# Kernel optimization log

Measured on AMD Instinct MI355X. Metric: run time of the kernel, lower is better.

The kernel has to match this reference:

```python
import jax, jax.numpy as jnp
import numpy as np

B = 65536   # batch
D = 15      # data_dim = 4**n_qubits - 1 (2 qubits)
DT = 0.01   # time step


def _pauli_s_const():
    # SU(4) structure constants from 2-qubit Pauli strings (identity excluded).
    I = np.eye(2, dtype=complex)
    X = np.array([[0, 1], [1, 0]], dtype=complex)
    Y = np.array([[0, -1j], [1j, 0]], dtype=complex)
    Z = np.array([[1, 0], [0, -1]], dtype=complex)
    sig = [I, X, Y, Z]
    P = np.stack([np.kron(a, b) for a in sig for b in sig][1:])  # [15,4,4]
    T = np.einsum('iab,jbc,kca->ijk', P, P, P)  # tr(Pi Pj Pk)
    f = (np.imag(T) / 4.0).astype(np.float32)  # antisymmetric
    d = (np.real(T) / 4.0).astype(np.float32)  # symmetric
    return f, d


def setup_inputs() -> dict:
    key = jax.random.key(0)
    ks = jax.random.split(key, 24)
    f, d = _pauli_s_const()

    def lin_w(k, o, i):
        return jax.random.normal(k, (o, i), jnp.float32) / np.sqrt(i)

    def lin_b(k, o):
        return 0.001 * jax.random.normal(k, (o,), jnp.float32)

    dims = [(2, 1), (4, 2), (4, 4), (D * D, 4)]
    inp = {
        't': jax.random.uniform(ks[0], (B,), jnp.float32),
        'x': jax.random.normal(ks[1], (B, D), jnp.float32),
        'omega': 0.001 * jax.random.normal(ks[2], (D,), jnp.float32),
        'f': jnp.asarray(f),
        'd': jnp.asarray(d),
    }
    kidx = 3
    for net in ('x', 'y'):
        for li, (o, i) in enumerate(dims, start=1):
            inp[f'w{net}{li}'] = lin_w(ks[kidx], o, i); kidx += 1
            inp[f'b{net}{li}'] = lin_b(ks[kidx], o); kidx += 1
    return inp


def _forward(t, x, wx1, bx1, wx2, bx2, wx3, bx3, wx4, bx4,
             wy1, by1, wy2, by2, wy3, by3, wy4, by4, omega, f, d):
    t1 = t[:, None]  # [B,1]

    def mlp(w1, b1, w2, b2, w3, b3, w4, b4):
        h = jax.nn.relu(t1 @ w1.T + b1)
        h = jax.nn.relu(h @ w2.T + b2)
        h = jax.nn.relu(h @ w3.T + b3)
        return (h @ w4.T + b4).reshape(-1, D, D)  # [B,D,D]

    vx = mlp(wx1, bx1, wx2, bx2, wx3, bx3, wx4, bx4)
    vy = mlp(wy1, by1, wy2, by2, wy3, by3, wy4, by4)

    c_re = jnp.einsum('ski,skj->sij', vx, vx) + jnp.einsum('ski,skj->sij', vy, vy)
    c_im = jnp.einsum('ski,skj->sij', vx, vy) - jnp.einsum('ski,skj->sij', vy, vx)

    # Hoist the batch-independent structure-constant contractions ([D,D,D,D], tiny).
    M_re = jnp.einsum('mjk,nik->mnij', f, f) + jnp.einsum('mik,njk->mnij', f, f)
    M_im = jnp.einsum('mik,njk->mnij', f, d) - jnp.einsum('mjk,nik->mnij', f, d)

    d_super = (-4.0) * jnp.einsum('mnij,sij->smn', M_re, c_re) \
              + 4.0 * jnp.einsum('mnij,sij->smn', M_im, c_im)  # [B,D,D]
    tr_id = -4.0 * jnp.einsum('imj,sij->sm', f, c_im)           # [B,D]
    h_comm = 4.0 * jnp.einsum('ijk,k->ji', f, omega)            # [D,D]

    bsz = t.shape[0]
    L = jnp.zeros((bsz, D + 1, D + 1), t.dtype)
    L = L.at[:, 1:, 1:].set(h_comm[None] + d_super)
    L = L.at[:, 1:, 0].set(tr_id)

    E = jax.scipy.linalg.expm(DT * L)  # batched Pade scaling-squaring, [B,D+1,D+1]
    # out = E[:,1:,0] + x @ E[:,1:,1:]^T  (per batch)
    return E[:, 1:, 0] + jnp.einsum('si,sji->sj', x, E[:, 1:, 1:])


def reference(t, x, omega, f, d,
              wx1, bx1, wx2, bx2, wx3, bx3, wx4, bx4,
              wy1, by1, wy2, by2, wy3, by3, wy4, by4):
    return _forward(t, x, wx1, bx1, wx2, bx2, wx3, bx3, wx4, bx4,
                    wy1, by1, wy2, by2, wy3, by3, wy4, by4, omega, f, d)
```

## Files before the change

### kernel.cpp

```cpp
#include <hip/hip_runtime.h>
#include <math.h>

#define DTC 0.01f
#define NZ 56
#define ZH 28
#define SSTR 260

__device__ float g_Wre[225*240];
__device__ float g_Wim[225*240];
__device__ float g_Pxx[15*225];
__device__ float g_Pyy[15*225];
__device__ float g_Cim[25*225];
__device__ float g_G  [NZ*256];

__constant__ int c_pa[15] = {0,0,0,0,0,1,1,1,1,2,2,2,3,3,4};
__constant__ int c_pb[15] = {0,1,2,3,4,1,2,3,4,2,3,4,3,4,4};

#define QPERM(ctrl_, v_) __int_as_float(__builtin_amdgcn_update_dpp( \
    __float_as_int(v_), __float_as_int(v_), (ctrl_), 0xF, 0xF, true))

__global__ void pk1(const float* __restrict__ f, const float* __restrict__ d,
                    const float* __restrict__ wx4, const float* __restrict__ bx4,
                    const float* __restrict__ wy4, const float* __restrict__ by4)
{
  const int b = blockIdx.x;
  const int i = b / 15, j = b % 15;
  const int t = threadIdx.x;

  if (t < 240) {
    float wre = 0.f, wim = 0.f;
    if (t < 225) {
      const int al = t / 15, be = t % 15;
      float sre = 0.f, sim = 0.f;
      for (int k = 0; k < 15; ++k) {
        const float faj = f[(al*15 + j)*15 + k];
        const float fai = f[(al*15 + i)*15 + k];
        const float fbi = f[(be*15 + i)*15 + k];
        const float fbj = f[(be*15 + j)*15 + k];
        const float dbj = d[(be*15 + j)*15 + k];
        const float dbi = d[(be*15 + i)*15 + k];
        sre += faj*fbi + fai*fbj;
        sim += fai*dbj - faj*dbi;
      }
      wre = -4.f*DTC*sre;
      wim =  4.f*DTC*sim;
    } else {
      const int al = t - 225;
      wim = -4.f*DTC*f[(i*15 + al)*15 + j];
    }
    g_Wre[b*240 + t] = wre;
    g_Wim[b*240 + t] = wim;
  }

  if (t < 55) {
    if (t < 30) {
      const int a  = c_pa[t % 15], bb = c_pb[t % 15];
      const float* w4 = (t < 15) ? wx4 : wy4;
      const float* b4 = (t < 15) ? bx4 : by4;
      float s1 = 0.f, s2 = 0.f;
      for (int k = 0; k < 15; ++k) {
        const int oi = k*15 + i, oj = k*15 + j;
        const float Aia = (a  < 4) ? w4[oi*4 + a ] : b4[oi];
        const float Ajb = (bb < 4) ? w4[oj*4 + bb] : b4[oj];
        const float Aib = (bb < 4) ? w4[oi*4 + bb] : b4[oi];
        const float Aja = (a  < 4) ? w4[oj*4 + a ] : b4[oj];
        s1 += Aia*Ajb;
        s2 += Aib*Aja;
      }
      const float v = (a == bb) ? s1 : (s1 + s2);
      if (t < 15) g_Pxx[t*225 + b] = v;
      else        g_Pyy[(t-15)*225 + b] = v;
    } else {
      const int tt = t - 30, a = tt / 5, bb = tt % 5;
      float s = 0.f;
      for (int k = 0; k < 15; ++k) {
        const int oi = k*15 + i, oj = k*15 + j;
        const float Axia = (a  < 4) ? wx4[oi*4 + a ] : bx4[oi];
        const float Ayjb = (bb < 4) ? wy4[oj*4 + bb] : by4[oj];
        const float Ayib = (bb < 4) ? wy4[oi*4 + bb] : by4[oi];
        const float Axja = (a  < 4) ? wx4[oj*4 + a ] : bx4[oj];
        s += Axia*Ayjb - Ayib*Axja;
      }
      g_Cim[tt*225 + b] = s;
    }
  }
}

__global__ void pk2(const float* __restrict__ f, const float* __restrict__ omega)
{
  const int z = blockIdx.x;
  const int t = threadIdx.x;
  __shared__ float Prow[225];
  const float* W = nullptr; const float* P = nullptr;
  if (z < 15)      { P = g_Pxx + z*225;        W = g_Wre; }
  else if (z < 30) { P = g_Pyy + (z-15)*225;   W = g_Wre; }
  else if (z < 55) { P = g_Cim + (z-30)*225;   W = g_Wim; }
  if (P && t < 225) Prow[t] = P[t];
  __syncthreads();

  const int r = t >> 4, c = t & 15;
  float g = 0.f;
  if (P && r > 0) {
    const int de = (c >= 1) ? ((r-1)*15 + (c-1)) : (225 + (r-1));
    for (int ij = 0; ij < 225; ++ij)
      g = fmaf(W[ij*240 + de], Prow[ij], g);
    if (z == 14 && c >= 1) {
      float hc = 0.f;
      for (int k = 0; k < 15; ++k)
        hc = fmaf(f[((c-1)*15 + (r-1))*15 + k], omega[k], hc);
      g += DTC * 4.f * hc;
    }
  }
  const int c4 = c >> 2;
  const int slot = (c4 + (r >> 1)) & 3;
  g_G[(z << 8) + (r << 4) + (slot << 2) + (c & 3)] = g;
}

__device__ __forceinline__ void gemm_half(float (&acc)[4][16],
                                          const float* __restrict__ Gt,
                                          const float* __restrict__ Zl,
                                          int half, int w, int p, int q)
{
  #pragma unroll 2
  for (int zt = 0; zt < ZH; ++zt) {
    const float4 zv = *(const float4*)&Zl[(half*ZH + zt)*64 + (w << 4) + (p << 2)];
    const float za[4] = {zv.x, zv.y, zv.z, zv.w};
    #pragma unroll
    for (int lc = 0; lc < 4; ++lc) {
      const int slot = (lc + (q >> 1)) & 3;
      const float4 gv = *(const float4*)&Gt[(zt << 8) + (q << 4) + (slot << 2)];
      const float gg[4] = {gv.x, gv.y, gv.z, gv.w};
      #pragma unroll
      for (int jj = 0; jj < 4; ++jj)
        #pragma unroll
        for (int cc = 0; cc < 4; ++cc)
          acc[jj][(lc << 2) + cc] = fmaf(za[jj], gg[cc], acc[jj][(lc << 2) + cc]);
    }
  }
}

__device__ __forceinline__ void mm16q(float (&C2)[4][16],
                                      const float (&A2)[4][16],
                                      const float (&B2)[4][16])
{
#define KSTEP(kk) { \
    float bk[16]; \
    _Pragma("unroll") \
    for (int c = 0; c < 16; ++c) bk[c] = QPERM((((kk) >> 2) * 0x55), B2[(kk) & 3][c]); \
    _Pragma("unroll") \
    for (int u = 0; u < 4; ++u) { \
      const float av = A2[u][kk]; \
      _Pragma("unroll") \
      for (int c = 0; c < 16; ++c) C2[u][c] = fmaf(av, bk[c], C2[u][c]); \
    } }
  KSTEP(1) KSTEP(2) KSTEP(3) KSTEP(4) KSTEP(5) KSTEP(6) KSTEP(7) KSTEP(8)
  KSTEP(9) KSTEP(10) KSTEP(11) KSTEP(12) KSTEP(13) KSTEP(14) KSTEP(15)
#undef KSTEP
}

__attribute__((amdgpu_waves_per_eu(2, 2)))
__global__ void __launch_bounds__(256)
mainker(const float* __restrict__ t_in, const float* __restrict__ x_in,
        const float* __restrict__ wx1, const float* __restrict__ bx1,
        const float* __restrict__ wx2, const float* __restrict__ bx2,
        const float* __restrict__ wx3, const float* __restrict__ bx3,
        const float* __restrict__ wy1, const float* __restrict__ by1,
        const float* __restrict__ wy2, const float* __restrict__ by2,
        const float* __restrict__ wy3, const float* __restrict__ by3,
        float* __restrict__ out, int B)
{
  __shared__ __align__(16) float S[64*SSTR];
  float* const Gt = S;
  float* const Zl = S + ZH*256;

  const int tid = threadIdx.x;
  const int w = tid >> 6;
  const int l = tid & 63;
  const int p = l & 3;
  const int q = l >> 2;

  for (int base = blockIdx.x*64; base < B; base += gridDim.x*64) {
    __syncthreads();

    #pragma unroll
    for (int ch = 0; ch < 7; ++ch) {
      const int off = (w*7 + ch)*256 + (l << 2);
      *(float4*)&Gt[off] = *(const float4*)&g_G[off];
    }
    if (p == 0) {
      const int zsmp = base + (w << 4) + q;
      const float tv = (zsmp < B) ? t_in[zsmp] : 0.f;
      float hx[5], hy[5];
      {
        const float a0 = fmaxf(fmaf(wx1[0], tv, bx1[0]), 0.f);
        const float a1 = fmaxf(fmaf(wx1[1], tv, bx1[1]), 0.f);
        float h2[4];
        #pragma unroll
        for (int o = 0; o < 4; ++o)
          h2[o] = fmaxf(wx2[o*2+0]*a0 + wx2[o*2+1]*a1 + bx2[o], 0.f);
        #pragma unroll
        for (int o = 0; o < 4; ++o)
          hx[o] = fmaxf(wx3[o*4+0]*h2[0] + wx3[o*4+1]*h2[1] +
                        wx3[o*4+2]*h2[2] + wx3[o*4+3]*h2[3] + bx3[o], 0.f);
        hx[4] = 1.f;
      }
      {
        const float a0 = fmaxf(fmaf(wy1[0], tv, by1[0]), 0.f);
        const float a1 = fmaxf(fmaf(wy1[1], tv, by1[1]), 0.f);
        float h2[4];
        #pragma unroll
        for (int o = 0; o < 4; ++o)
          h2[o] = fmaxf(wy2[o*2+0]*a0 + wy2[o*2+1]*a1 + by2[o], 0.f);
        #pragma unroll
        for (int o = 0; o < 4; ++o)
          hy[o] = fmaxf(wy3[o*4+0]*h2[0] + wy3[o*4+1]*h2[1] +
                        wy3[o*4+2]*h2[2] + wy3[o*4+3]*h2[3] + by3[o], 0.f);
        hy[4] = 1.f;
      }
      const int col = (w << 4) + q;
      constexpr int zb[5] = {0,5,9,12,14};
      #pragma unroll
      for (int a = 0; a < 5; ++a)
        #pragma unroll
        for (int b2 = a; b2 < 5; ++b2) {
          Zl[(zb[a] + b2 - a)*64 + col]      = hx[a]*hx[b2];
          Zl[(15 + zb[a] + b2 - a)*64 + col] = hy[a]*hy[b2];
        }
      #pragma unroll
      for (int a = 0; a < 5; ++a)
        #pragma unroll
        for (int b2 = 0; b2 < 5; ++b2)
          Zl[(30 + a*5 + b2)*64 + col] = hx[a]*hy[b2];
      Zl[55*64 + col] = 0.f;
    }
    __syncthreads();

    float acc[4][16];
    #pragma unroll
    for (int jj = 0; jj < 4; ++jj)
      #pragma unroll
      for (int cc = 0; cc < 16; ++cc) acc[jj][cc] = 0.f;

    gemm_half(acc, Gt, Zl, 0, w, p, q);
    __syncthreads();
    #pragma unroll
    for (int ch = 0; ch < 7; ++ch) {
      const int off = (w*7 + ch)*256 + (l << 2);
      *(float4*)&Gt[off] = *(const float4*)&g_G[ZH*256 + off];
    }
    __syncthreads();
    gemm_half(acc, Gt, Zl, 1, w, p, q);
    __syncthreads();

    {
      float* Ms0 = S + (w*16 + p*4)*SSTR + q*16;
      #pragma unroll
      for (int jj = 0; jj < 4; ++jj)
        #pragma unroll
        for (int c4 = 0; c4 < 4; ++c4)
          *(float4*)&Ms0[jj*SSTR + (c4 << 2)] =
            make_float4(acc[jj][(c4<<2)+0], acc[jj][(c4<<2)+1],
                        acc[jj][(c4<<2)+2], acc[jj][(c4<<2)+3]);
    }
    __syncthreads();

    const int smp = base + (w << 4) + q;
    const float* const Msamp = S + ((w << 4) + q)*SSTR;

    float Mo[4][16];
    #pragma unroll
    for (int u = 0; u < 4; ++u)
      #pragma unroll
      for (int c4 = 0; c4 < 4; ++c4) {
        const float4 v = *(const float4*)&Msamp[(p*4 + u)*16 + (c4 << 2)];
        Mo[u][(c4<<2)+0] = v.x; Mo[u][(c4<<2)+1] = v.y;
        Mo[u][(c4<<2)+2] = v.z; Mo[u][(c4<<2)+3] = v.w;
      }

    float nrm = 0.f;
    #pragma unroll
    for (int u = 0; u < 4; ++u) {
      float rs = 0.f;
      #pragma unroll
      for (int c = 0; c < 16; ++c) rs += fabsf(Mo[u][c]);
      nrm = fmaxf(nrm, rs);
    }
    nrm = fmaxf(nrm, QPERM(0xB1, nrm));
    nrm = fmaxf(nrm, QPERM(0x4E, nrm));
    int sq = 0;
    if (nrm > 0.5f) sq = (int)ceilf(log2f(nrm * 2.f));
    sq = (sq < 0) ? 0 : ((sq > 40) ? 40 : sq);
    const float sc = exp2f((float)(-sq));
    #pragma unroll
    for (int u = 0; u < 4; ++u)
      #pragma unroll
      for (int c = 0; c < 16; ++c) Mo[u][c] *= sc;

    float P[4][16];
    #pragma unroll
    for (int u = 0; u < 4; ++u)
      #pragma unroll
      for (int c = 0; c < 16; ++c) P[u][c] = Mo[u][c] * (1.f/6.f);

    #pragma unroll 1
    for (int s7 = 0; s7 < 5; ++s7) {
      float C[4][16];
      #pragma unroll
      for (int u = 0; u < 4; ++u)
        #pragma unroll
        for (int c = 0; c < 16; ++c) C[u][c] = Mo[u][c];
      mm16q(C, P, Mo);
      const float ik = 1.f / (float)(5 - s7);
      #pragma unroll
      for (int u = 0; u < 4; ++u)
        #pragma unroll
        for (int c = 0; c < 16; ++c) P[u][c] = C[u][c] * ik;
    }

    #pragma unroll 1
    for (int it2 = 0; it2 < sq; ++it2) {
      float C[4][16];
      #pragma unroll
      for (int u = 0; u < 4; ++u)
        #pragma unroll
        for (int c = 0; c < 16; ++c) C[u][c] = 2.f*P[u][c];
      mm16q(C, P, P);
      #pragma unroll
      for (int u = 0; u < 4; ++u)
        #pragma unroll
        for (int c = 0; c < 16; ++c) P[u][c] = C[u][c];
    }

    if (smp < B) {
      float xv[15];
      #pragma unroll
      for (int i2 = 0; i2 < 15; ++i2) xv[i2] = x_in[smp*15 + i2];
      #pragma unroll
      for (int u = 0; u < 4; ++u) {
        const int row = (p << 2) + u;
        if (row >= 1) {
          float o = P[u][0];
          #pragma unroll
          for (int i2 = 0; i2 < 15; ++i2) o = fmaf(xv[i2], P[u][1 + i2], o);
          o += xv[row - 1];
          out[smp*15 + (row - 1)] = o;
        }
      }
    }
  }
}

extern "C" void kernel_launch(void* const* d_in, const int* in_sizes, int n_in,
                              void* d_out, int out_size, void* d_ws, size_t ws_size,
                              hipStream_t stream)
{
  const float* t   = (const float*)d_in[0];
  const float* x   = (const float*)d_in[1];
  const float* om  = (const float*)d_in[2];
  const float* f   = (const float*)d_in[3];
  const float* dd  = (const float*)d_in[4];
  const float* wx1 = (const float*)d_in[5];  const float* bx1 = (const float*)d_in[6];
  const float* wx2 = (const float*)d_in[7];  const float* bx2 = (const float*)d_in[8];
  const float* wx3 = (const float*)d_in[9];  const float* bx3 = (const float*)d_in[10];
  const float* wx4 = (const float*)d_in[11]; const float* bx4 = (const float*)d_in[12];
  const float* wy1 = (const float*)d_in[13]; const float* by1 = (const float*)d_in[14];
  const float* wy2 = (const float*)d_in[15]; const float* by2 = (const float*)d_in[16];
  const float* wy3 = (const float*)d_in[17]; const float* by3 = (const float*)d_in[18];
  const float* wy4 = (const float*)d_in[19]; const float* by4 = (const float*)d_in[20];
  float* out = (float*)d_out;
  const int B = in_sizes[0];

  hipLaunchKernelGGL(pk1, dim3(225), dim3(256), 0, stream, f, dd, wx4, bx4, wy4, by4);
  hipLaunchKernelGGL(pk2, dim3(56),  dim3(256), 0, stream, f, om);
  hipLaunchKernelGGL(mainker, dim3(1024), dim3(256), 0, stream,
                     t, x, wx1, bx1, wx2, bx2, wx3, bx3,
                     wy1, by1, wy2, by2, wy3, by3, out, B);
}
```

Measured before the change: 244.2 us.

## Split matrix-exponential work across 8 lanes per sample with swizzle broadcasts

The Taylor/squaring stage of the 16x16 matrix exponential now gives each sample 8 lanes holding 2 rows each, instead of 4 lanes holding 4 rows each. Each wave processes its samples in two passes over the LDS tile. The cross-lane operand broadcast switches from DPP quad permutes to ds_swizzle, and sched barriers are added between k-steps. Launch bounds replace the waves_per_eu attribute. The aim is to cut the per-thread register footprint so more waves can run, at the cost of LDS-path swizzle latency and serialising sample groups.

New measurement: 336.2 us. +37.7%, slower.

```diff
diff --git a/kernel.cpp b/kernel.cpp
--- a/kernel.cpp
+++ b/kernel.cpp
@@ -18,6 +18,8 @@
 
 #define QPERM(ctrl_, v_) __int_as_float(__builtin_amdgcn_update_dpp( \
     __float_as_int(v_), __float_as_int(v_), (ctrl_), 0xF, 0xF, true))
+#define SWZF(imm_, v_) __int_as_float(__builtin_amdgcn_ds_swizzle( \
+    __float_as_int(v_), (imm_)))
 
 __global__ void pk1(const float* __restrict__ f, const float* __restrict__ d,
                     const float* __restrict__ wx4, const float* __restrict__ bx4,
@@ -139,27 +141,28 @@
   }
 }
 
-__device__ __forceinline__ void mm16q(float (&C2)[4][16],
-                                      const float (&A2)[4][16],
-                                      const float (&B2)[4][16])
+__device__ __forceinline__ void mm8s(float (&C2)[2][16],
+                                     const float (&A2)[2][16],
+                                     const float (&B2)[2][16])
 {
 #define KSTEP(kk) { \
     float bk[16]; \
     _Pragma("unroll") \
-    for (int c = 0; c < 16; ++c) bk[c] = QPERM((((kk) >> 2) * 0x55), B2[(kk) & 3][c]); \
+    for (int c = 0; c < 16; ++c) \
+      bk[c] = SWZF(((((kk) >> 1) << 5) | 0x18), B2[(kk) & 1][c]); \
     _Pragma("unroll") \
-    for (int u = 0; u < 4; ++u) { \
+    for (int u = 0; u < 2; ++u) { \
       const float av = A2[u][kk]; \
       _Pragma("unroll") \
       for (int c = 0; c < 16; ++c) C2[u][c] = fmaf(av, bk[c], C2[u][c]); \
-    } }
+    } \
+    __builtin_amdgcn_sched_barrier(0); }
   KSTEP(1) KSTEP(2) KSTEP(3) KSTEP(4) KSTEP(5) KSTEP(6) KSTEP(7) KSTEP(8)
   KSTEP(9) KSTEP(10) KSTEP(11) KSTEP(12) KSTEP(13) KSTEP(14) KSTEP(15)
 #undef KSTEP
 }
 
-__attribute__((amdgpu_waves_per_eu(2, 2)))
-__global__ void __launch_bounds__(256)
+__global__ void __launch_bounds__(256, 2)
 mainker(const float* __restrict__ t_in, const float* __restrict__ x_in,
         const float* __restrict__ wx1, const float* __restrict__ bx1,
         const float* __restrict__ wx2, const float* __restrict__ bx2,
@@ -178,6 +181,8 @@
   const int l = tid & 63;
   const int p = l & 3;
   const int q = l >> 2;
+  const int g8 = l >> 3;
+  const int e8 = l & 7;
 
   for (int base = blockIdx.x*64; base < B; base += gridDim.x*64) {
     __syncthreads();
@@ -264,86 +269,91 @@
     }
     __syncthreads();
 
-    const int smp = base + (w << 4) + q;
-    const float* const Msamp = S + ((w << 4) + q)*SSTR;
-
-    float Mo[4][16];
-    #pragma unroll
-    for (int u = 0; u < 4; ++u)
-      #pragma unroll
-      for (int c4 = 0; c4 < 4; ++c4) {
-        const float4 v = *(const float4*)&Msamp[(p*4 + u)*16 + (c4 << 2)];
-        Mo[u][(c4<<2)+0] = v.x; Mo[u][(c4<<2)+1] = v.y;
-        Mo[u][(c4<<2)+2] = v.z; Mo[u][(c4<<2)+3] = v.w;
-      }
-
-    float nrm = 0.f;
-    #pragma unroll
-    for (int u = 0; u < 4; ++u) {
-      float rs = 0.f;
-      #pragma unroll
-      for (int c = 0; c < 16; ++c) rs += fabsf(Mo[u][c]);
-      nrm = fmaxf(nrm, rs);
-    }
-    nrm = fmaxf(nrm, QPERM(0xB1, nrm));
-    nrm = fmaxf(nrm, QPERM(0x4E, nrm));
-    int sq = 0;
-    if (nrm > 0.5f) sq = (int)ceilf(log2f(nrm * 2.f));
-    sq = (sq < 0) ? 0 : ((sq > 40) ? 40 : sq);
-    const float sc = exp2f((float)(-sq));
-    #pragma unroll
-    for (int u = 0; u < 4; ++u)
-      #pragma unroll
-      for (int c = 0; c < 16; ++c) Mo[u][c] *= sc;
-
-    float P[4][16];
-    #pragma unroll
-    for (int u = 0; u < 4; ++u)
-      #pragma unroll
-      for (int c = 0; c < 16; ++c) P[u][c] = Mo[u][c] * (1.f/6.f);
-
     #pragma unroll 1
-    for (int s7 = 0; s7 < 5; ++s7) {
-      float C[4][16];
-      #pragma unroll
-      for (int u = 0; u < 4; ++u)
-        #pragma unroll
-        for (int c = 0; c < 16; ++c) C[u][c] = Mo[u][c];
-      mm16q(C, P, Mo);
-      const float ik = 1.f / (float)(5 - s7);
-      #pragma unroll
-      for (int u = 0; u < 4; ++u)
-        #pragma unroll
-        for (int c = 0; c < 16; ++c) P[u][c] = C[u][c] * ik;
-    }
-
-    #pragma unroll 1
-    for (int it2 = 0; it2 < sq; ++it2) {
-      float C[4][16];
-      #pragma unroll
-      for (int u = 0; u < 4; ++u)
-        #pragma unroll
-        for (int c = 0; c < 16; ++c) C[u][c] = 2.f*P[u][c];
-      mm16q(C, P, P);
-      #pragma unroll
-      for (int u = 0; u < 4; ++u)
-        #pragma unroll
-        for (int c = 0; c < 16; ++c) P[u][c] = C[u][c];
-    }
-
-    if (smp < B) {
-      float xv[15];
-      #pragma unroll
-      for (int i2 = 0; i2 < 15; ++i2) xv[i2] = x_in[smp*15 + i2];
-      #pragma unroll
-      for (int u = 0; u < 4; ++u) {
-        const int row = (p << 2) + u;
-        if (row >= 1) {
-          float o = P[u][0];
+    for (int ex = 0; ex < 2; ++ex) {
+      const int slot = (ex << 5) + (w << 3) + g8;
+      const int smp = base + slot;
+      const float* const Msamp = S + slot*SSTR;
+
+      float Mo[2][16];
+      #pragma unroll
+      for (int u = 0; u < 2; ++u)
+        #pragma unroll
+        for (int c4 = 0; c4 < 4; ++c4) {
+          const float4 v = *(const float4*)&Msamp[((e8 << 1) + u)*16 + (c4 << 2)];
+          Mo[u][(c4<<2)+0] = v.x; Mo[u][(c4<<2)+1] = v.y;
+          Mo[u][(c4<<2)+2] = v.z; Mo[u][(c4<<2)+3] = v.w;
+        }
+
+      float nrm = 0.f;
+      #pragma unroll
+      for (int u = 0; u < 2; ++u) {
+        float rs = 0.f;
+        #pragma unroll
+        for (int c = 0; c < 16; ++c) rs += fabsf(Mo[u][c]);
+        nrm = fmaxf(nrm, rs);
+      }
+      nrm = fmaxf(nrm, SWZF(0x041F, nrm));
+      nrm = fmaxf(nrm, SWZF(0x081F, nrm));
+      nrm = fmaxf(nrm, SWZF(0x101F, nrm));
+      int sq = 0;
+      if (nrm > 0.5f) sq = (int)ceilf(log2f(nrm * 2.f));
+      sq = (sq < 0) ? 0 : ((sq > 40) ? 40 : sq);
+      const float sc = exp2f((float)(-sq));
+      #pragma unroll
+      for (int u = 0; u < 2; ++u)
+        #pragma unroll
+        for (int c = 0; c < 16; ++c) Mo[u][c] *= sc;
+
+      float P[2][16];
+      #pragma unroll
+      for (int u = 0; u < 2; ++u)
+        #pragma unroll
+        for (int c = 0; c < 16; ++c) P[u][c] = Mo[u][c] * (1.f/6.f);
+
+      #pragma unroll 1
+      for (int s7 = 0; s7 < 5; ++s7) {
+        float C[2][16];
+        #pragma unroll
+        for (int u = 0; u < 2; ++u)
           #pragma unroll
-          for (int i2 = 0; i2 < 15; ++i2) o = fmaf(xv[i2], P[u][1 + i2], o);
-          o += xv[row - 1];
-          out[smp*15 + (row - 1)] = o;
+          for (int c = 0; c < 16; ++c) C[u][c] = Mo[u][c];
+        mm8s(C, P, Mo);
+        const float ik = 1.f / (float)(5 - s7);
+        #pragma unroll
+        for (int u = 0; u < 2; ++u)
+          #pragma unroll
+          for (int c = 0; c < 16; ++c) P[u][c] = C[u][c] * ik;
+      }
+
+      #pragma unroll 1
+      for (int it2 = 0; it2 < sq; ++it2) {
+        float C[2][16];
+        #pragma unroll
+        for (int u = 0; u < 2; ++u)
+          #pragma unroll
+          for (int c = 0; c < 16; ++c) C[u][c] = 2.f*P[u][c];
+        mm8s(C, P, P);
+        #pragma unroll
+        for (int u = 0; u < 2; ++u)
+          #pragma unroll
+          for (int c = 0; c < 16; ++c) P[u][c] = C[u][c];
+      }
+
+      if (smp < B) {
+        float xv[15];
+        #pragma unroll
+        for (int i2 = 0; i2 < 15; ++i2) xv[i2] = x_in[smp*15 + i2];
+        #pragma unroll
+        for (int u = 0; u < 2; ++u) {
+          const int row = (e8 << 1) + u;
+          if (row >= 1) {
+            float o = P[u][0];
+            #pragma unroll
+            for (int i2 = 0; i2 < 15; ++i2) o = fmaf(xv[i2], P[u][1 + i2], o);
+            o += xv[row - 1];
+            out[smp*15 + (row - 1)] = o;
+          }
         }
       }
     }
```
